# Performance work log

Measured on AMD Instinct MI355X. Metric: run time of the kernel, lower is better.

## Reference

```python
import jax, jax.numpy as jnp
import numpy as np

CAPACITY = 1024


def setup_inputs() -> dict:
    T, H, I, E, K = 2048, 1024, 1408, 8, 2
    key = jax.random.key(0)
    k0, k1, k2, k3, k4 = jax.random.split(key, 5)
    hidden_states = jax.random.normal(k0, (T, H), dtype=jnp.float32)
    w1 = jax.random.normal(k1, (E, 2 * I, H), dtype=jnp.float32) * 0.02  # [gate; up]
    w2 = jax.random.normal(k2, (E, H, I), dtype=jnp.float32) * 0.02
    topk_weights = jax.random.uniform(k3, (T, K), dtype=jnp.float32)
    topk_ids = jax.random.randint(k4, (T, K), 0, E, dtype=jnp.int32)
    return {"hidden_states": hidden_states, "w1": w1, "w2": w2,
            "topk_weights": topk_weights, "topk_ids": topk_ids}


def reference(hidden_states, w1, w2, topk_weights, topk_ids):
    # MoE: prepare(dispatch) -> grouped expert GEMM (silu-gated MLP) -> finalize(combine)
    T, H = hidden_states.shape
    E = w1.shape[0]
    I = w2.shape[2]
    K = topk_ids.shape[1]
    C = CAPACITY

    # ---- prepare: dispatch token copies to per-expert buffers ----
    flat_ids = topk_ids.reshape(-1)                       # (T*K,)
    onehot = jax.nn.one_hot(flat_ids, E, dtype=jnp.int32)  # (T*K, E)
    cs = jnp.cumsum(onehot, axis=0)                        # running per-expert counts
    pos = jnp.take_along_axis(cs, flat_ids[:, None], axis=1)[:, 0] - 1  # slot in expert buffer
    keep = pos < C
    pos_c = jnp.where(keep, pos, 0)

    x_flat = jnp.repeat(hidden_states, K, axis=0)          # (T*K, H)
    x_e = jnp.zeros((E, C, H), dtype=hidden_states.dtype)
    x_e = x_e.at[flat_ids, pos_c].add(jnp.where(keep[:, None], x_flat, 0.0))

    # ---- grouped expert GEMM: silu(gate) * up, then down-proj ----
    h = jnp.einsum('ech,eoh->eco', x_e, w1)                # (E, C, 2I)
    gate, up = h[..., :I], h[..., I:]
    act = jax.nn.silu(gate) * up                           # (E, C, I)
    y = jnp.einsum('eci,ehi->ech', act, w2)                # (E, C, H)

    # ---- finalize: gather back, apply router weights, reduce over top-k ----
    y_flat = y[flat_ids, pos_c] * (keep[:, None].astype(y.dtype)) \
             * topk_weights.reshape(-1, 1)                 # (T*K, H)
    out = y_flat.reshape(T, K, H).sum(axis=1)              # (T, H)
    return out.astype(hidden_states.dtype)
```

## Files before the change

kernel.cpp:

```cpp
#include <hip/hip_runtime.h>

#define NE 8
#define CAP 1024
#define HD 1024
#define ID 1408
#define TT 2048

typedef __attribute__((ext_vector_type(8))) short bf16x8;
typedef __attribute__((ext_vector_type(4))) float f32x4;
typedef unsigned short u16;
typedef unsigned int u32;
typedef unsigned long long u64;

__device__ __forceinline__ u16 f2bf(float f) {
  u32 u = __float_as_uint(f);
  u = (u + 0x7fffu + ((u >> 16) & 1u)) >> 16;
  return (u16)u;
}

__device__ __forceinline__ bf16x8 pack8(float4 a, float4 b) {
  bf16x8 r;
  r[0] = (short)f2bf(a.x); r[1] = (short)f2bf(a.y);
  r[2] = (short)f2bf(a.z); r[3] = (short)f2bf(a.w);
  r[4] = (short)f2bf(b.x); r[5] = (short)f2bf(b.y);
  r[6] = (short)f2bf(b.z); r[7] = (short)f2bf(b.w);
  return r;
}

__device__ __forceinline__ void async_cp16(const void* g, void* l) {
  __builtin_amdgcn_global_load_lds(
      (const __attribute__((address_space(1))) u32*)g,
      (__attribute__((address_space(3))) u32*)l, 16, 0, 0);
}

#define W1ROWS (NE * 2 * ID)
#define XBLK (TT * HD / 4 / 256)
#define OZB (TT * HD / 4 / 256)
__global__ __launch_bounds__(256) void prep_kernel(
    const float4* __restrict__ w1, ushort4* __restrict__ bw1,
    const float4* __restrict__ x, ushort4* __restrict__ bx,
    const int* __restrict__ ids, int* __restrict__ rowmap,
    int* __restrict__ counts, float4* __restrict__ outz) {
  int b = blockIdx.x;
  int tid = threadIdx.x;
  if (b == 0) {
    __shared__ unsigned char ids_s[TT * 2];
    __shared__ int sc[256][NE + 1];
    for (int i = tid; i < TT * 2; i += 256) ids_s[i] = (unsigned char)ids[i];
    __syncthreads();
    int base = tid * 16;
    u64 own64 = 0;
#pragma unroll
    for (int j = 0; j < 16; ++j) own64 += 1ull << (ids_s[base + j] * 8);
    int own[NE];
#pragma unroll
    for (int e = 0; e < NE; ++e) {
      own[e] = (int)((own64 >> (e * 8)) & 0xff);
      sc[tid][e] = own[e];
    }
    __syncthreads();
    for (int off = 1; off < 256; off <<= 1) {
      int v[NE];
      if (tid >= off) {
#pragma unroll
        for (int e = 0; e < NE; ++e) v[e] = sc[tid - off][e];
      }
      __syncthreads();
      if (tid >= off) {
#pragma unroll
        for (int e = 0; e < NE; ++e) sc[tid][e] += v[e];
      }
      __syncthreads();
    }
    if (tid == 255) {
#pragma unroll
      for (int e = 0; e < NE; ++e) counts[e] = sc[255][e] < CAP ? sc[255][e] : CAP;
    }
    int excl[NE];
#pragma unroll
    for (int e = 0; e < NE; ++e) excl[e] = sc[tid][e] - own[e];
    __syncthreads();
#pragma unroll
    for (int e = 0; e < NE; ++e) sc[tid][e] = excl[e];
#pragma unroll
    for (int j = 0; j < 16; ++j) {
      int f = base + j;
      int e = ids_s[f];
      int p = sc[tid][e]++;
      if (p < CAP) rowmap[e * CAP + p] = f;
    }
    return;
  }
  int bb = b - 1;
  if (bb < W1ROWS) {
    int n = bb % (2 * ID);
    int e = bb / (2 * ID);
    int j = (n < ID) ? n : (n - ID);
    int np = (j >> 4) * 32 + (j & 15) + ((n < ID) ? 0 : 16);
    float4 v = w1[((size_t)e * 2 * ID + n) * (HD / 4) + tid];
    ushort4 o;
    o.x = f2bf(v.x); o.y = f2bf(v.y); o.z = f2bf(v.z); o.w = f2bf(v.w);
    bw1[((size_t)e * 2 * ID + np) * (HD / 4) + tid] = o;
  } else if (bb < W1ROWS + XBLK) {
    size_t i = (size_t)(bb - W1ROWS) * 256 + tid;
    float4 v = x[i];
    ushort4 o;
    o.x = f2bf(v.x); o.y = f2bf(v.y); o.z = f2bf(v.z); o.w = f2bf(v.w);
    bx[i] = o;
  } else {
    size_t i = (size_t)(bb - W1ROWS - XBLK) * 256 + tid;
    float4 z = {0.f, 0.f, 0.f, 0.f};
    outz[i] = z;
  }
}

#define G1BUF 24576
__global__ __launch_bounds__(256) void gemm1_kernel(
    const u16* __restrict__ A, const u16* __restrict__ B, u16* __restrict__ Hb,
    const int* __restrict__ rowmap, const int* __restrict__ counts,
    const float4* __restrict__ W2, bf16x8* __restrict__ bw2) {
  int bid = blockIdx.x;
  int tid = threadIdx.x;
  int grp = bid >> 3, sub = bid & 7;
  int q7 = grp / 7, r7 = grp - q7 * 7;
  if (r7 == 2 || r7 == 5) {
    int r = (q7 * 2 + (r7 == 5 ? 1 : 0)) * 8 + sub;
#pragma unroll
    for (int k2 = 0; k2 < 4; ++k2) {
      size_t base4 = ((size_t)r * 4 + k2) * 1024;
      float4 v0 = W2[base4 + tid * 2];
      float4 v1 = W2[base4 + tid * 2 + 1];
      float4 v2 = W2[base4 + 512 + tid * 2];
      float4 v3 = W2[base4 + 512 + tid * 2 + 1];
      bf16x8* dst = bw2 + base4 / 2;
      dst[tid] = pack8(v0, v1);
      dst[256 + tid] = pack8(v2, v3);
    }
    return;
  }
  int tg = q7 * 5 + r7 - (r7 > 2 ? 1 : 0) - (r7 > 5 ? 1 : 0);
  int e = sub;
  int my = tg % 10;
  int n0 = (tg / 10) * 128;
  int count = counts[e];
  int lane = tid & 63, wid = tid >> 6;
  int wm = wid >> 1, wn = wid & 1;
  int q = lane >> 4, lm = lane & 15;

  __shared__ __align__(16) char sm[3 * G1BUF];

  int rloc = tid >> 3;
  int chs = ((tid & 7) ^ (rloc & 7)) * 8;
  const u16* bP[4];
#pragma unroll
  for (int i = 0; i < 4; ++i)
    bP[i] = B + ((size_t)e * 2 * ID + n0 + rloc + 32 * i) * HD + chs;

#define STAGE1(base, kt)                                             \
  do {                                                               \
    int ko_ = (kt) * 64;                                             \
    char* sb_ = (base);                                              \
    async_cp16(aP[0] + ko_, sb_ + (0 * 256 + tid) * 16);             \
    async_cp16(aP[1] + ko_, sb_ + (1 * 256 + tid) * 16);             \
    async_cp16(bP[0] + ko_, sb_ + 8192 + (0 * 256 + tid) * 16);      \
    async_cp16(bP[1] + ko_, sb_ + 8192 + (1 * 256 + tid) * 16);      \
    async_cp16(bP[2] + ko_, sb_ + 8192 + (2 * 256 + tid) * 16);      \
    async_cp16(bP[3] + ko_, sb_ + 8192 + (3 * 256 + tid) * 16);      \
  } while (0)

  for (int m0 = my * 64; m0 < count; m0 += 640) {
    const u16* aP[2];
#pragma unroll
    for (int i = 0; i < 2; ++i) {
      int gr = m0 + rloc + 32 * i;
      int f = (gr < count) ? rowmap[e * CAP + gr] : 0;
      aP[i] = A + (size_t)(f >> 1) * HD + chs;
    }

    f32x4 zero = {0.f, 0.f, 0.f, 0.f};
    f32x4 acc[2][4];
#pragma unroll
    for (int mi = 0; mi < 2; ++mi)
#pragma unroll
      for (int ni = 0; ni < 4; ++ni) acc[mi][ni] = zero;

    STAGE1(sm, 0);
    STAGE1(sm + G1BUF, 1);
    int p = 0, pn2 = 2;
    for (int kt = 0; kt < HD / 64; ++kt) {
      if (kt == HD / 64 - 1)
        asm volatile("s_waitcnt vmcnt(0)\ns_barrier" ::: "memory");
      else
        asm volatile("s_waitcnt vmcnt(6)\ns_barrier" ::: "memory");
      const char* sb = sm + p * G1BUF;
      if (kt + 2 < HD / 64) STAGE1(sm + pn2 * G1BUF, kt + 2);
#pragma unroll
      for (int s = 0; s < 2; ++s) {
        int cs = ((s * 4 + q) ^ (lm & 7)) * 16;
        bf16x8 af[2], bfr[4];
#pragma unroll
        for (int mi = 0; mi < 2; ++mi)
          af[mi] = *(const bf16x8*)(sb + (wm * 32 + mi * 16 + lm) * 128 + cs);
#pragma unroll
        for (int ni = 0; ni < 4; ++ni)
          bfr[ni] = *(const bf16x8*)(sb + 8192 + (wn * 64 + ni * 16 + lm) * 128 + cs);
        __builtin_amdgcn_s_setprio(1);
#pragma unroll
        for (int mi = 0; mi < 2; ++mi)
#pragma unroll
          for (int ni = 0; ni < 4; ++ni)
            acc[mi][ni] = __builtin_amdgcn_mfma_f32_16x16x32_bf16(af[mi], bfr[ni], acc[mi][ni], 0, 0, 0);
        __builtin_amdgcn_s_setprio(0);
      }
      p = (p == 2) ? 0 : p + 1;
      pn2 = (pn2 == 2) ? 0 : pn2 + 1;
    }
    __syncthreads();

    u16* smOut = (u16*)sm;
#pragma unroll
    for (int mi = 0; mi < 2; ++mi) {
#pragma unroll
      for (int k = 0; k < 2; ++k) {
        int colL = wn * 32 + k * 16 + lm;
#pragma unroll
        for (int r = 0; r < 4; ++r) {
          float g2 = acc[mi][2 * k][r];
          float u = acc[mi][2 * k + 1][r];
          float a = g2 / (1.f + __expf(-g2)) * u;
          int row = wm * 32 + mi * 16 + q * 4 + r;
          smOut[row * 72 + colL] = f2bf(a);
        }
      }
    }
    __syncthreads();
    {
      int row = tid >> 2, seg = tid & 3;
      const u16* sp = smOut + row * 72 + seg * 16;
      bf16x8 v0 = *(const bf16x8*)sp;
      bf16x8 v1 = *(const bf16x8*)(sp + 8);
      u16* dp = Hb + ((size_t)e * CAP + m0 + row) * ID + (n0 >> 1) + seg * 16;
      *(bf16x8*)dp = v0;
      *(bf16x8*)(dp + 8) = v1;
    }
    __syncthreads();
  }
}

#define G2BUF 16384
__global__ __launch_bounds__(256) void gemm2_kernel(
    const u16* __restrict__ A, const u16* __restrict__ B, float* __restrict__ out,
    const int* __restrict__ rowmap, const int* __restrict__ counts,
    const float* __restrict__ tw) {
  int idx = blockIdx.x;
  int e = idx & 7;
  int tg = idx >> 3;
  int my = tg % 10;
  int n0 = (tg / 10) * 64;
  int count = counts[e];
  int tid = threadIdx.x;
  int lane = tid & 63, wid = tid >> 6;
  int wm = wid >> 1, wn = wid & 1;
  int q = lane >> 4, lm = lane & 15;

  __shared__ __align__(16) char sm[3 * G2BUF];

  int rloc = tid >> 3;
  int chs = ((tid & 7) ^ (rloc & 7)) * 8;
  const u16* bP[2];
#pragma unroll
  for (int i = 0; i < 2; ++i)
    bP[i] = B + ((size_t)e * HD + n0 + rloc + 32 * i) * ID + chs;

#define STAGE2(base, kt)                                             \
  do {                                                               \
    int ko_ = (kt) * 64;                                             \
    char* sb_ = (base);                                              \
    async_cp16(aP[0] + ko_, sb_ + (0 * 256 + tid) * 16);             \
    async_cp16(aP[1] + ko_, sb_ + (1 * 256 + tid) * 16);             \
    async_cp16(bP[0] + ko_, sb_ + 8192 + (0 * 256 + tid) * 16);      \
    async_cp16(bP[1] + ko_, sb_ + 8192 + (1 * 256 + tid) * 16);      \
  } while (0)

  for (int m0 = my * 64; m0 < count; m0 += 640) {
    const u16* aP[2];
#pragma unroll
    for (int i = 0; i < 2; ++i)
      aP[i] = A + ((size_t)e * CAP + m0 + rloc + 32 * i) * ID + chs;

    f32x4 zero = {0.f, 0.f, 0.f, 0.f};
    f32x4 acc[2][2];
#pragma unroll
    for (int mi = 0; mi < 2; ++mi)
#pragma unroll
      for (int ni = 0; ni < 2; ++ni) acc[mi][ni] = zero;

    STAGE2(sm, 0);
    STAGE2(sm + G2BUF, 1);
    int p = 0, pn2 = 2;
    for (int kt = 0; kt < ID / 64; ++kt) {
      if (kt == ID / 64 - 1)
        asm volatile("s_waitcnt vmcnt(0)\ns_barrier" ::: "memory");
      else
        asm volatile("s_waitcnt vmcnt(4)\ns_barrier" ::: "memory");
      const char* sb = sm + p * G2BUF;
      if (kt + 2 < ID / 64) STAGE2(sm + pn2 * G2BUF, kt + 2);
#pragma unroll
      for (int s = 0; s < 2; ++s) {
        int cs = ((s * 4 + q) ^ (lm & 7)) * 16;
        bf16x8 af[2], bfr[2];
#pragma unroll
        for (int mi = 0; mi < 2; ++mi)
          af[mi] = *(const bf16x8*)(sb + (wm * 32 + mi * 16 + lm) * 128 + cs);
#pragma unroll
        for (int ni = 0; ni < 2; ++ni)
          bfr[ni] = *(const bf16x8*)(sb + 8192 + (wn * 32 + ni * 16 + lm) * 128 + cs);
        __builtin_amdgcn_s_setprio(1);
#pragma unroll
        for (int mi = 0; mi < 2; ++mi)
#pragma unroll
          for (int ni = 0; ni < 2; ++ni)
            acc[mi][ni] = __builtin_amdgcn_mfma_f32_16x16x32_bf16(af[mi], bfr[ni], acc[mi][ni], 0, 0, 0);
        __builtin_amdgcn_s_setprio(0);
      }
      p = (p == 2) ? 0 : p + 1;
      pn2 = (pn2 == 2) ? 0 : pn2 + 1;
    }

#pragma unroll
    for (int mi = 0; mi < 2; ++mi) {
#pragma unroll
      for (int r = 0; r < 4; ++r) {
        int grow = m0 + wm * 32 + mi * 16 + q * 4 + r;
        if (grow < count) {
          int f = rowmap[e * CAP + grow];
          float w = tw[f];
          int t = f >> 1;
#pragma unroll
          for (int ni = 0; ni < 2; ++ni) {
            int col = n0 + wn * 32 + ni * 16 + lm;
            atomicAdd(&out[(size_t)t * HD + col], w * acc[mi][ni][r]);
          }
        }
      }
    }
    __syncthreads();
  }
}

extern "C" void kernel_launch(void* const* d_in, const int* in_sizes, int n_in,
                              void* d_out, int out_size, void* d_ws, size_t ws_size,
                              hipStream_t stream) {
  const float* hidden = (const float*)d_in[0];
  const float* w1 = (const float*)d_in[1];
  const float* w2 = (const float*)d_in[2];
  const float* tw = (const float*)d_in[3];
  const int* ids = (const int*)d_in[4];
  float* out = (float*)d_out;

  char* p = (char*)d_ws;
  auto alloc = [&](size_t b) { char* r = p; p += (b + 255) & ~(size_t)255; return r; };
  u16* bw1 = (u16*)alloc((size_t)NE * 2 * ID * HD * 2);
  u16* bw2 = (u16*)alloc((size_t)NE * HD * ID * 2);
  u16* bx = (u16*)alloc((size_t)TT * HD * 2);
  u16* hbuf = (u16*)alloc((size_t)NE * CAP * ID * 2);
  int* rowmap = (int*)alloc((size_t)NE * CAP * 4);
  int* counts = (int*)alloc((size_t)NE * 4);

  prep_kernel<<<1 + W1ROWS + XBLK + OZB, 256, 0, stream>>>(
      (const float4*)w1, (ushort4*)bw1, (const float4*)hidden, (ushort4*)bx,
      ids, rowmap, counts, (float4*)out);

  gemm1_kernel<<<308 * 8, 256, 0, stream>>>(
      bx, bw1, hbuf, rowmap, counts, (const float4*)w2, (bf16x8*)bw2);

  gemm2_kernel<<<8 * 10 * 16, 256, 0, stream>>>(
      hbuf, bw2, out, rowmap, counts, tw);
}
```

Measured before the change: 250.6 us.

## Move output zeroing into gemm1 filler blocks and widen gemm2 N-tile to 128

Output zeroing moves out of the prep kernel and into spare blocks of gemm1, which now interleaves 3 conversion/zero blocks per 10 groups alongside the GEMM tiles. gemm2 doubles its N tile from 64 to 128 columns per block, with more B loads per stage, 8 accumulators per wave and half as many blocks. The goal is to shorten the prep kernel's critical path and to reuse each A tile across twice as many output columns. In exchange gemm2 uses more LDS and registers per block and launches fewer blocks, which may lower occupancy and parallelism.

Result: slower. 258.1 us (+3.0%).

```diff
diff --git a/kernel.cpp b/kernel.cpp
--- a/kernel.cpp
+++ b/kernel.cpp
@@ -35,12 +35,11 @@
 
 #define W1ROWS (NE * 2 * ID)
 #define XBLK (TT * HD / 4 / 256)
-#define OZB (TT * HD / 4 / 256)
 __global__ __launch_bounds__(256) void prep_kernel(
     const float4* __restrict__ w1, ushort4* __restrict__ bw1,
     const float4* __restrict__ x, ushort4* __restrict__ bx,
     const int* __restrict__ ids, int* __restrict__ rowmap,
-    int* __restrict__ counts, float4* __restrict__ outz) {
+    int* __restrict__ counts) {
   int b = blockIdx.x;
   int tid = threadIdx.x;
   if (b == 0) {
@@ -101,16 +100,12 @@
     ushort4 o;
     o.x = f2bf(v.x); o.y = f2bf(v.y); o.z = f2bf(v.z); o.w = f2bf(v.w);
     bw1[((size_t)e * 2 * ID + np) * (HD / 4) + tid] = o;
-  } else if (bb < W1ROWS + XBLK) {
+  } else {
     size_t i = (size_t)(bb - W1ROWS) * 256 + tid;
     float4 v = x[i];
     ushort4 o;
     o.x = f2bf(v.x); o.y = f2bf(v.y); o.z = f2bf(v.z); o.w = f2bf(v.w);
     bx[i] = o;
-  } else {
-    size_t i = (size_t)(bb - W1ROWS - XBLK) * 256 + tid;
-    float4 z = {0.f, 0.f, 0.f, 0.f};
-    outz[i] = z;
   }
 }
 
@@ -118,27 +113,38 @@
 __global__ __launch_bounds__(256) void gemm1_kernel(
     const u16* __restrict__ A, const u16* __restrict__ B, u16* __restrict__ Hb,
     const int* __restrict__ rowmap, const int* __restrict__ counts,
-    const float4* __restrict__ W2, bf16x8* __restrict__ bw2) {
+    const float4* __restrict__ W2, bf16x8* __restrict__ bw2,
+    float4* __restrict__ outz) {
   int bid = blockIdx.x;
   int tid = threadIdx.x;
   int grp = bid >> 3, sub = bid & 7;
-  int q7 = grp / 7, r7 = grp - q7 * 7;
-  if (r7 == 2 || r7 == 5) {
-    int r = (q7 * 2 + (r7 == 5 ? 1 : 0)) * 8 + sub;
-#pragma unroll
-    for (int k2 = 0; k2 < 4; ++k2) {
-      size_t base4 = ((size_t)r * 4 + k2) * 1024;
-      float4 v0 = W2[base4 + tid * 2];
-      float4 v1 = W2[base4 + tid * 2 + 1];
-      float4 v2 = W2[base4 + 512 + tid * 2];
-      float4 v3 = W2[base4 + 512 + tid * 2 + 1];
-      bf16x8* dst = bw2 + base4 / 2;
-      dst[tid] = pack8(v0, v1);
-      dst[256 + tid] = pack8(v2, v3);
+  int sup = grp / 10, r10 = grp - sup * 10;
+  if (r10 == 2 || r10 == 5 || r10 == 8) {
+    int which = (r10 == 2) ? 0 : (r10 == 5) ? 1 : 2;
+    int r = sup * 3 + which;
+    if (r < 88) {
+      int rb = r * 8 + sub;
+#pragma unroll
+      for (int k2 = 0; k2 < 4; ++k2) {
+        size_t base4 = ((size_t)rb * 4 + k2) * 1024;
+        float4 v0 = W2[base4 + tid * 2];
+        float4 v1 = W2[base4 + tid * 2 + 1];
+        float4 v2 = W2[base4 + 512 + tid * 2];
+        float4 v3 = W2[base4 + 512 + tid * 2 + 1];
+        bf16x8* dst = bw2 + base4 / 2;
+        dst[tid] = pack8(v0, v1);
+        dst[256 + tid] = pack8(v2, v3);
+      }
+    } else {
+      size_t base = (size_t)((r - 88) * 8 + sub) * 8192;
+      float4 z = {0.f, 0.f, 0.f, 0.f};
+#pragma unroll
+      for (int i2 = 0; i2 < 32; ++i2) outz[base + i2 * 256 + tid] = z;
     }
     return;
   }
-  int tg = q7 * 5 + r7 - (r7 > 2 ? 1 : 0) - (r7 > 5 ? 1 : 0);
+  int tg = sup * 7 + r10 - (r10 > 2 ? 1 : 0) - (r10 > 5 ? 1 : 0) - (r10 > 8 ? 1 : 0);
+  if (tg >= 220) return;
   int e = sub;
   int my = tg % 10;
   int n0 = (tg / 10) * 128;
@@ -247,7 +253,7 @@
   }
 }
 
-#define G2BUF 16384
+#define G2BUF 24576
 __global__ __launch_bounds__(256) void gemm2_kernel(
     const u16* __restrict__ A, const u16* __restrict__ B, float* __restrict__ out,
     const int* __restrict__ rowmap, const int* __restrict__ counts,
@@ -256,7 +262,7 @@
   int e = idx & 7;
   int tg = idx >> 3;
   int my = tg % 10;
-  int n0 = (tg / 10) * 64;
+  int n0 = (tg / 10) * 128;
   int count = counts[e];
   int tid = threadIdx.x;
   int lane = tid & 63, wid = tid >> 6;
@@ -267,9 +273,9 @@
 
   int rloc = tid >> 3;
   int chs = ((tid & 7) ^ (rloc & 7)) * 8;
-  const u16* bP[2];
-#pragma unroll
-  for (int i = 0; i < 2; ++i)
+  const u16* bP[4];
+#pragma unroll
+  for (int i = 0; i < 4; ++i)
     bP[i] = B + ((size_t)e * HD + n0 + rloc + 32 * i) * ID + chs;
 
 #define STAGE2(base, kt)                                             \
@@ -280,6 +286,8 @@
     async_cp16(aP[1] + ko_, sb_ + (1 * 256 + tid) * 16);             \
     async_cp16(bP[0] + ko_, sb_ + 8192 + (0 * 256 + tid) * 16);      \
     async_cp16(bP[1] + ko_, sb_ + 8192 + (1 * 256 + tid) * 16);      \
+    async_cp16(bP[2] + ko_, sb_ + 8192 + (2 * 256 + tid) * 16);      \
+    async_cp16(bP[3] + ko_, sb_ + 8192 + (3 * 256 + tid) * 16);      \
   } while (0)
 
   for (int m0 = my * 64; m0 < count; m0 += 640) {
@@ -289,11 +297,11 @@
       aP[i] = A + ((size_t)e * CAP + m0 + rloc + 32 * i) * ID + chs;
 
     f32x4 zero = {0.f, 0.f, 0.f, 0.f};
-    f32x4 acc[2][2];
+    f32x4 acc[2][4];
 #pragma unroll
     for (int mi = 0; mi < 2; ++mi)
 #pragma unroll
-      for (int ni = 0; ni < 2; ++ni) acc[mi][ni] = zero;
+      for (int ni = 0; ni < 4; ++ni) acc[mi][ni] = zero;
 
     STAGE2(sm, 0);
     STAGE2(sm + G2BUF, 1);
@@ -302,24 +310,24 @@
       if (kt == ID / 64 - 1)
         asm volatile("s_waitcnt vmcnt(0)\ns_barrier" ::: "memory");
       else
-        asm volatile("s_waitcnt vmcnt(4)\ns_barrier" ::: "memory");
+        asm volatile("s_waitcnt vmcnt(6)\ns_barrier" ::: "memory");
       const char* sb = sm + p * G2BUF;
       if (kt + 2 < ID / 64) STAGE2(sm + pn2 * G2BUF, kt + 2);
 #pragma unroll
       for (int s = 0; s < 2; ++s) {
         int cs = ((s * 4 + q) ^ (lm & 7)) * 16;
-        bf16x8 af[2], bfr[2];
+        bf16x8 af[2], bfr[4];
 #pragma unroll
         for (int mi = 0; mi < 2; ++mi)
           af[mi] = *(const bf16x8*)(sb + (wm * 32 + mi * 16 + lm) * 128 + cs);
 #pragma unroll
-        for (int ni = 0; ni < 2; ++ni)
-          bfr[ni] = *(const bf16x8*)(sb + 8192 + (wn * 32 + ni * 16 + lm) * 128 + cs);
+        for (int ni = 0; ni < 4; ++ni)
+          bfr[ni] = *(const bf16x8*)(sb + 8192 + (wn * 64 + ni * 16 + lm) * 128 + cs);
         __builtin_amdgcn_s_setprio(1);
 #pragma unroll
         for (int mi = 0; mi < 2; ++mi)
 #pragma unroll
-          for (int ni = 0; ni < 2; ++ni)
+          for (int ni = 0; ni < 4; ++ni)
             acc[mi][ni] = __builtin_amdgcn_mfma_f32_16x16x32_bf16(af[mi], bfr[ni], acc[mi][ni], 0, 0, 0);
         __builtin_amdgcn_s_setprio(0);
       }
@@ -337,8 +345,8 @@
           float w = tw[f];
           int t = f >> 1;
 #pragma unroll
-          for (int ni = 0; ni < 2; ++ni) {
-            int col = n0 + wn * 32 + ni * 16 + lm;
+          for (int ni = 0; ni < 4; ++ni) {
+            int col = n0 + wn * 64 + ni * 16 + lm;
             atomicAdd(&out[(size_t)t * HD + col], w * acc[mi][ni][r]);
           }
         }
@@ -367,13 +375,14 @@
   int* rowmap = (int*)alloc((size_t)NE * CAP * 4);
   int* counts = (int*)alloc((size_t)NE * 4);
 
-  prep_kernel<<<1 + W1ROWS + XBLK + OZB, 256, 0, stream>>>(
+  prep_kernel<<<1 + W1ROWS + XBLK, 256, 0, stream>>>(
       (const float4*)w1, (ushort4*)bw1, (const float4*)hidden, (ushort4*)bx,
-      ids, rowmap, counts, (float4*)out);
-
-  gemm1_kernel<<<308 * 8, 256, 0, stream>>>(
-      bx, bw1, hbuf, rowmap, counts, (const float4*)w2, (bf16x8*)bw2);
-
-  gemm2_kernel<<<8 * 10 * 16, 256, 0, stream>>>(
+      ids, rowmap, counts);
+
+  gemm1_kernel<<<320 * 8, 256, 0, stream>>>(
+      bx, bw1, hbuf, rowmap, counts, (const float4*)w2, (bf16x8*)bw2,
+      (float4*)out);
+
+  gemm2_kernel<<<8 * 10 * 8, 256, 0, stream>>>(
       hbuf, bw2, out, rowmap, counts, tw);
 }
```
